# Performance work log

Hardware: AMD Instinct MI355X
Metric: run time of the kernel (lower is better)

## Reference

```python
import jax, jax.numpy as jnp
import numpy as np

B, SQ, SKV = 4, 2048, 2048
IN_Q, IN_KV = 1024, 1024
H, D = 16, 64            # num_heads, hidden_channels (per-head dim)
OUT = 1024
ROPE_BASE = 4096.0


def _rope(x, base):
    # x: (..., items, D). Interleaved rotate-half RoPE over last dim.
    d = x.shape[-1]
    s = x.shape[-2]
    inv_freq = base ** (-jnp.arange(0, d, 2, dtype=x.dtype) / d)      # (D/2,)
    ang = jnp.arange(s, dtype=x.dtype)[:, None] * inv_freq[None, :]   # (S, D/2)
    cos = jnp.repeat(jnp.cos(ang), 2, axis=-1)                        # (S, D)
    sin = jnp.repeat(jnp.sin(ang), 2, axis=-1)
    xp = x.reshape(x.shape[:-1] + (d // 2, 2))
    x_rot = jnp.stack([-xp[..., 1], xp[..., 0]], axis=-1).reshape(x.shape)
    return x * cos + x_rot * sin


def setup_inputs() -> dict:
    key = jax.random.key(0)
    ks = jax.random.split(key, 8)
    sc = 0.02
    return {
        "q": jax.random.normal(ks[0], (B, SQ, IN_Q), jnp.float32),
        "kv": jax.random.normal(ks[1], (B, SKV, IN_KV), jnp.float32),
        # weights stored (in, out): y = x @ W + b  (equiv. to torch Linear)
        "Wq": jax.random.normal(ks[2], (IN_Q, H * D), jnp.float32) * sc,
        "bq": jnp.zeros((H * D,), jnp.float32),
        "Wkv": jax.random.normal(ks[3], (IN_KV, 2 * D), jnp.float32) * sc,
        "bkv": jnp.zeros((2 * D,), jnp.float32),
        "Wo": jax.random.normal(ks[4], (H * D, OUT), jnp.float32) * sc,
        "bo": jnp.zeros((OUT,), jnp.float32),
    }


def reference(q, kv, Wq, bq, Wkv, bkv, Wo, bo):
    # Q projection -> (B, H, SQ, D)
    qh = (q @ Wq + bq).reshape(B, SQ, H, D).transpose(0, 2, 1, 3)
    # KV projection (multi-query: single shared K/V head) -> (B, SKV, D) each
    kvp = kv @ Wkv + bkv
    k, v = kvp[..., :D], kvp[..., D:]
    # Rotary positional encoding on the item axis
    qh = _rope(qh, ROPE_BASE)
    k = _rope(k, ROPE_BASE)
    # Scaled dot-product attention with broadcast single-head K/V (MQA)
    scale = 1.0 / jnp.sqrt(jnp.asarray(D, qh.dtype))
    scores = jnp.einsum("bhqd,bkd->bhqk", qh, k) * scale   # (B,H,SQ,SKV)
    attn = jax.nn.softmax(scores, axis=-1)
    h = jnp.einsum("bhqk,bkd->bhqd", attn, v)              # (B,H,SQ,D)
    # Merge heads and output projection
    h = h.transpose(0, 2, 1, 3).reshape(B, SQ, H * D)
    return h @ Wo + bo
```

## Files before the change

### kernel.cpp

```cpp
#include <hip/hip_runtime.h>
#include <math.h>

typedef __bf16 bf16;
typedef __bf16 bf16x4 __attribute__((ext_vector_type(4)));
typedef __bf16 bf16x8 __attribute__((ext_vector_type(8)));
typedef float floatx4 __attribute__((ext_vector_type(4)));

#define MFMA16(a, b, c) __builtin_amdgcn_mfma_f32_16x16x32_bf16(a, b, c, 0, 0, 0)

#if __has_builtin(__builtin_amdgcn_exp2f)
#define EXP2F(x) __builtin_amdgcn_exp2f(x)
#else
#define EXP2F(x) exp2f(x)
#endif

constexpr int Bc = 4, SQc = 2048, SKVc = 2048, Hc = 16, Dc = 64;
#define QSCALE 0.18033688011112042f

__device__ __forceinline__ void glds16(const bf16* g, bf16* lds_base, int lane) {
#if __has_builtin(__builtin_amdgcn_global_load_lds)
  __builtin_amdgcn_global_load_lds(
      (const __attribute__((address_space(1))) void*)g,
      (__attribute__((address_space(3))) void*)lds_base, 16, 0, 0);
#else
  *(bf16x8*)(lds_base + 8 * lane) = *(const bf16x8*)g;
#endif
}

__device__ __forceinline__ void cvt_body(const float* __restrict__ in,
                                         bf16* __restrict__ out, int blk,
                                         int tid) {
  const size_t i = ((size_t)blk * 256 + tid) * 4;
  const float4 v = *(const float4*)&in[i];
  bf16x4 o = {(bf16)v.x, (bf16)v.y, (bf16)v.z, (bf16)v.w};
  *(bf16x4*)&out[i] = o;
}

__device__ __forceinline__ void transpose_body(const float* __restrict__ in,
                                               bf16* __restrict__ out, int K,
                                               int N, int bx, int by, int tid,
                                               bf16 (*T)[72]) {
  const int n0 = bx * 64, k0 = by * 64;
  const int tr = tid >> 4, tc4 = (tid & 15) * 4;
#pragma unroll
  for (int i = 0; i < 4; i++) {
    const int k = tr + 16 * i;
    const float4 v = *(const float4*)&in[(size_t)(k0 + k) * N + n0 + tc4];
    T[tc4 + 0][k] = (bf16)v.x;
    T[tc4 + 1][k] = (bf16)v.y;
    T[tc4 + 2][k] = (bf16)v.z;
    T[tc4 + 3][k] = (bf16)v.w;
  }
  __syncthreads();
  const int nr = tid >> 2, kc = (tid & 3) * 8;
#pragma unroll
  for (int hf = 0; hf < 2; hf++)
    *(bf16x8*)&out[(size_t)(n0 + nr) * K + k0 + kc + 32 * hf] =
        *(const bf16x8*)&T[nr][kc + 32 * hf];
}

__global__ void prep(const float* __restrict__ q, const float* __restrict__ kv,
                     const float* __restrict__ Wq, const float* __restrict__ Wkv,
                     const float* __restrict__ Wo, bf16* __restrict__ qbf,
                     bf16* __restrict__ kvbf, bf16* __restrict__ WqT,
                     bf16* __restrict__ WkvT, bf16* __restrict__ WoT,
                     float2* __restrict__ rtab) {
  __shared__ bf16 T[64][72];
  const int blk = blockIdx.x, tid = threadIdx.x;
  if (blk < 8192) {
    cvt_body(q, qbf, blk, tid);
  } else if (blk < 16384) {
    cvt_body(kv, kvbf, blk - 8192, tid);
  } else if (blk < 16640) {
    const int i = blk - 16384;
    transpose_body(Wq, WqT, 1024, 1024, i & 15, i >> 4, tid, T);
  } else if (blk < 16672) {
    const int i = blk - 16640;
    transpose_body(Wkv, WkvT, 1024, 128, i & 1, i >> 1, tid, T);
  } else if (blk < 16928) {
    const int i = blk - 16672;
    transpose_body(Wo, WoT, 1024, 1024, i & 15, i >> 4, tid, T);
  } else {
    const int i = (blk - 16928) * 256 + tid;
    const int pos = i >> 5, f = i & 31;
    const float ang = (float)pos * exp2f(-0.375f * (float)f);
    float sn, cs;
    sincosf(ang, &sn, &cs);
    rtab[i] = make_float2(cs, sn);
  }
}

__device__ __forceinline__ void gemm_kloop(const bf16* __restrict__ A,
                                           const bf16* __restrict__ BT, int m0,
                                           int n0, int tid, int wave, int lane,
                                           int m, int g, bf16* As, bf16* Bs,
                                           floatx4 (*acc)[2], int mq, int nq) {
  const int r_ = tid >> 3, p_ = tid & 7;
  const bf16* pA[4];
  const bf16* pB[2];
#pragma unroll
  for (int q = 0; q < 4; q++) {
    const int r = r_ + q * 32;
    const int s = p_ ^ (r & 7);
    pA[q] = &A[(size_t)(m0 + r) * 1024 + 8 * s];
    if (q < 2) pB[q] = &BT[(size_t)(n0 + r) * 1024 + 8 * s];
  }

  for (int k0 = 0; k0 < 1024; k0 += 64) {
    __syncthreads();
#pragma unroll
    for (int q = 0; q < 4; q++)
      glds16(pA[q] + k0, &As[(q * 4 + wave) * 512], lane);
#pragma unroll
    for (int q = 0; q < 2; q++)
      glds16(pB[q] + k0, &Bs[(q * 4 + wave) * 512], lane);
    __syncthreads();

    bf16x8 bb[2][2];
#pragma unroll
    for (int j = 0; j < 2; j++) {
      const int row = nq + 16 * j + m;
#pragma unroll
      for (int kh = 0; kh < 2; kh++)
        bb[j][kh] = *(const bf16x8*)&Bs[row * 64 + 8 * ((g + 4 * kh) ^ (row & 7))];
    }
#pragma unroll
    for (int i = 0; i < 4; i++) {
      const int row = mq + 16 * i + m;
      const bf16x8 a0 = *(const bf16x8*)&As[row * 64 + 8 * (g ^ (row & 7))];
      const bf16x8 a1 = *(const bf16x8*)&As[row * 64 + 8 * ((g + 4) ^ (row & 7))];
#pragma unroll
      for (int j = 0; j < 2; j++) {
        acc[i][j] = MFMA16(a0, bb[j][0], acc[i][j]);
        acc[i][j] = MFMA16(a1, bb[j][1], acc[i][j]);
      }
    }
  }
}

__global__ __launch_bounds__(256, 4) void gemm_qkv(
    const bf16* __restrict__ qA, const bf16* __restrict__ qBT,
    const float* __restrict__ qb, const bf16* __restrict__ kvA,
    const bf16* __restrict__ kvBT, const float* __restrict__ kvb,
    const float2* __restrict__ tab, bf16* __restrict__ qh,
    bf16* __restrict__ kko, bf16* __restrict__ vto) {
  __shared__ bf16 As[128 * 64];
  __shared__ bf16 Bs[64 * 64];

  const int tid = threadIdx.x, lane = tid & 63, wave = tid >> 6;
  const int m = lane & 15, g = lane >> 4;
  const int m0 = blockIdx.x * 128;
  const bool isQ = (blockIdx.y < 16);
  const int n0 = isQ ? blockIdx.y * 64 : (blockIdx.y - 16) * 64;
  const bf16* A = isQ ? qA : kvA;
  const bf16* BT = isQ ? qBT : kvBT;
  const float* bias = isQ ? qb : kvb;
  const int mq = (wave >> 1) * 64, nq = (wave & 1) * 32;

  floatx4 z = {0.f, 0.f, 0.f, 0.f};
  floatx4 acc[4][2];
#pragma unroll
  for (int i = 0; i < 4; i++)
#pragma unroll
    for (int j = 0; j < 2; j++) acc[i][j] = z;

  gemm_kloop(A, BT, m0, n0, tid, wave, lane, m, g, As, Bs, acc, mq, nq);

  const int rq = 4 * g;
#pragma unroll
  for (int j = 0; j < 2; j++) {
    const int col = n0 + nq + 16 * j + m;
    const float bv = bias[col];
#pragma unroll
    for (int i = 0; i < 4; i++) {
#pragma unroll
      for (int r = 0; r < 4; r++) {
        const int row = m0 + mq + 16 * i + rq + r;
        float v = acc[i][j][r] + bv;
        const float vp = __shfl_xor(v, 1);
        if (isQ) {
          const int d = col & 63, hh = col >> 6;
          const int pos = row & (SQc - 1), b = row >> 11;
          const float2 cssn = tab[pos * 32 + (d >> 1)];
          const float res = (d & 1) ? (v * cssn.x + vp * cssn.y)
                                    : (v * cssn.x - vp * cssn.y);
          qh[(((size_t)(b * Hc + hh) * SQc) + pos) * Dc + d] = (bf16)(res * QSCALE);
        } else {
          const int pos = row & (SKVc - 1), b = row >> 11;
          const size_t fb = (size_t)b * (SKVc * Dc);
          if (col < 64) {
            const int d = col;
            const float2 cssn = tab[pos * 32 + (d >> 1)];
            const float res = (d & 1) ? (v * cssn.x + vp * cssn.y)
                                      : (v * cssn.x - vp * cssn.y);
            const int kc = (pos >> 4) * 2 + (d >> 5);
            const int kl = ((d >> 3) & 3) * 16 + (pos & 15);
            kko[fb + (size_t)kc * 512 + kl * 8 + (d & 7)] = (bf16)res;
          } else {
            const int d = col - 64;
            const int vc = (pos >> 6) * 8 + (d >> 4) * 2 + ((pos >> 5) & 1);
            const int vl = ((pos >> 3) & 3) * 16 + (d & 15);
            vto[fb + (size_t)vc * 512 + vl * 8 + (pos & 7)] = (bf16)v;
          }
        }
      }
    }
  }
}

__global__ __launch_bounds__(256, 4) void gemm_out(
    const bf16* __restrict__ A, const bf16* __restrict__ BT,
    const float* __restrict__ bias, float* __restrict__ out) {
  __shared__ bf16 As[128 * 64];
  __shared__ bf16 Bs[64 * 64];

  const int tid = threadIdx.x, lane = tid & 63, wave = tid >> 6;
  const int m = lane & 15, g = lane >> 4;
  const int m0 = blockIdx.x * 128, n0 = blockIdx.y * 64;
  const int mq = (wave >> 1) * 64, nq = (wave & 1) * 32;

  floatx4 z = {0.f, 0.f, 0.f, 0.f};
  floatx4 acc[4][2];
#pragma unroll
  for (int i = 0; i < 4; i++)
#pragma unroll
    for (int j = 0; j < 2; j++) acc[i][j] = z;

  gemm_kloop(A, BT, m0, n0, tid, wave, lane, m, g, As, Bs, acc, mq, nq);

  const int rq = 4 * g;
#pragma unroll
  for (int j = 0; j < 2; j++) {
    const int col = n0 + nq + 16 * j + m;
    const float bv = bias[col];
#pragma unroll
    for (int i = 0; i < 4; i++)
#pragma unroll
      for (int r = 0; r < 4; r++) {
        const int row = m0 + mq + 16 * i + rq + r;
        out[(size_t)row * 1024 + col] = acc[i][j][r] + bv;
      }
  }
}

__global__ __launch_bounds__(512, 4) void attn_v5(
    const bf16* __restrict__ qh, const bf16* __restrict__ kk,
    const bf16* __restrict__ vt, bf16* __restrict__ hout) {
  const int bid = blockIdx.x;
  const int qt = bid & 7, h = (bid >> 3) & 15, b = bid >> 7;
  const int tid = threadIdx.x, lane = tid & 63, wave = tid >> 6;
  const int m = lane & 15, g = lane >> 4;

  __shared__ bf16 Kb[2][4096];
  __shared__ bf16 Vb[4096];
  __shared__ bf16 Pb[8][2][16][68];

  const int q0 = qt * 256 + wave * 32;
  const bf16* qp = qh + (((size_t)(b * Hc + h) * SQc) + q0 + m) * Dc + 8 * g;
  bf16x8 bq[2][2];
#pragma unroll
  for (int s = 0; s < 2; s++) {
    bq[s][0] = *(const bf16x8*)(qp + (size_t)(16 * s) * Dc);
    bq[s][1] = *(const bf16x8*)(qp + (size_t)(16 * s) * Dc + 32);
  }

  const bf16 one = (bf16)1.0f;
  const bf16x8 ones = {one, one, one, one, one, one, one, one};

  floatx4 z = {0.f, 0.f, 0.f, 0.f};
  floatx4 accO[2][4];
  floatx4 lacc[2] = {z, z};
#pragma unroll
  for (int s = 0; s < 2; s++)
#pragma unroll
    for (int t = 0; t < 4; t++) accO[s][t] = z;

  const size_t fb = (size_t)b * (SKVc * Dc);
  const bf16* kg = kk + fb + 8 * lane;
  const bf16* vg = vt + fb + 8 * lane;

  glds16(kg + (size_t)wave * 512, &Kb[0][wave * 512], lane);
  __syncthreads();

  for (int it = 0; it < 32; ++it) {
    const int cur = it & 1;
    if (it) __syncthreads();
    glds16(vg + (size_t)(it * 8 + wave) * 512, &Vb[wave * 512], lane);
    if (it + 1 < 32)
      glds16(kg + (size_t)((it + 1) * 8 + wave) * 512, &Kb[cur ^ 1][wave * 512],
             lane);

    bf16x8 kfr[4][2];
#pragma unroll
    for (int c = 0; c < 4; c++) {
      kfr[c][0] = *(const bf16x8*)&Kb[cur][(2 * c + 0) * 512 + 8 * lane];
      kfr[c][1] = *(const bf16x8*)&Kb[cur][(2 * c + 1) * 512 + 8 * lane];
    }
#pragma unroll
    for (int s = 0; s < 2; s++) {
#pragma unroll
      for (int c = 0; c < 4; c++) {
        floatx4 sv = MFMA16(kfr[c][0], bq[s][0], z);
        sv = MFMA16(kfr[c][1], bq[s][1], sv);
        bf16x4 pk = {(bf16)EXP2F(sv[0]), (bf16)EXP2F(sv[1]), (bf16)EXP2F(sv[2]),
                     (bf16)EXP2F(sv[3])};
        *(bf16x4*)&Pb[wave][s][m][16 * c + 4 * g] = pk;
      }
    }
    __syncthreads();

    bf16x8 vf[4][2];
#pragma unroll
    for (int t = 0; t < 4; t++) {
      vf[t][0] = *(const bf16x8*)&Vb[(2 * t + 0) * 512 + 8 * lane];
      vf[t][1] = *(const bf16x8*)&Vb[(2 * t + 1) * 512 + 8 * lane];
    }
    __builtin_amdgcn_s_setprio(1);
#pragma unroll
    for (int s = 0; s < 2; s++) {
      const bf16x8 pa0 = *(const bf16x8*)&Pb[wave][s][m][8 * g];
      const bf16x8 pa1 = *(const bf16x8*)&Pb[wave][s][m][32 + 8 * g];
      lacc[s] = MFMA16(pa0, ones, lacc[s]);
      lacc[s] = MFMA16(pa1, ones, lacc[s]);
#pragma unroll
      for (int t = 0; t < 4; t++) {
        accO[s][t] = MFMA16(pa0, vf[t][0], accO[s][t]);
        accO[s][t] = MFMA16(pa1, vf[t][1], accO[s][t]);
      }
    }
    __builtin_amdgcn_s_setprio(0);
  }

#pragma unroll
  for (int s = 0; s < 2; s++) {
    floatx4 inv;
#pragma unroll
    for (int r = 0; r < 4; r++) inv[r] = 1.0f / lacc[s][r];
#pragma unroll
    for (int t = 0; t < 4; t++)
#pragma unroll
      for (int r = 0; r < 4; r++) {
        const int qrow = q0 + 16 * s + 4 * g + r;
        hout[((size_t)(b * SQc + qrow)) * (Hc * Dc) + h * Dc + 16 * t + m] =
            (bf16)(accO[s][t][r] * inv[r]);
      }
  }
}

extern "C" void kernel_launch(void* const* d_in, const int* in_sizes, int n_in,
                              void* d_out, int out_size, void* d_ws, size_t ws_size,
                              hipStream_t stream) {
  const float* q = (const float*)d_in[0];
  const float* kv = (const float*)d_in[1];
  const float* Wq = (const float*)d_in[2];
  const float* bq = (const float*)d_in[3];
  const float* Wkv = (const float*)d_in[4];
  const float* bkv = (const float*)d_in[5];
  const float* Wo = (const float*)d_in[6];
  const float* bo = (const float*)d_in[7];

  char* ws = (char*)d_ws;
  bf16* qbf = (bf16*)ws;
  bf16* kvbf = (bf16*)(ws + ((size_t)16 << 20));
  bf16* WqT = (bf16*)(ws + ((size_t)32 << 20));
  bf16* WkvT = (bf16*)(ws + ((size_t)34 << 20));
  float2* rtab = (float2*)(ws + ((size_t)34 << 20) + ((size_t)256 << 10));
  bf16* WoT = (bf16*)(ws + ((size_t)35 << 20));
  bf16* qh = (bf16*)(ws + ((size_t)37 << 20));
  bf16* kk = (bf16*)(ws + ((size_t)53 << 20));
  bf16* vt = (bf16*)(ws + ((size_t)54 << 20));
  bf16* hh = qbf;

  prep<<<17184, 256, 0, stream>>>(q, kv, Wq, Wkv, Wo, qbf, kvbf, WqT, WkvT, WoT,
                                  rtab);
  gemm_qkv<<<dim3(64, 18), 256, 0, stream>>>(qbf, WqT, bq, kvbf, WkvT, bkv, rtab,
                                             qh, kk, vt);
  attn_v5<<<Bc * Hc * (SQc / 256), 512, 0, stream>>>(qh, kk, vt, hh);
  gemm_out<<<dim3(64, 16), 256, 0, stream>>>(hh, WoT, bo, (float*)d_out);
}
```

Baseline: 261.5 us.

## Enlarge GEMM tiles to 256x64 with K-step 128 and 512-thread blocks

Both projection GEMMs now use 256-row by 64-column block tiles with a K depth of 128 per stage and 8 waves per block. Each wave owns 32 rows and all 64 columns, with a 16-wide XOR swizzle in LDS. This halves the number of K-loop barriers and raises the reuse of each B tile, so global-to-LDS traffic per FLOP drops. In exchange LDS use grows to 80KB per block and the grid shrinks to 576 and 512 blocks, which lowers occupancy and may leave CUs idle.

```diff
diff --git a/kernel.cpp b/kernel.cpp
--- a/kernel.cpp
+++ b/kernel.cpp
@@ -94,88 +94,80 @@
                                            const bf16* __restrict__ BT, int m0,
                                            int n0, int tid, int wave, int lane,
                                            int m, int g, bf16* As, bf16* Bs,
-                                           floatx4 (*acc)[2], int mq, int nq) {
-  const int r_ = tid >> 3, p_ = tid & 7;
-  const bf16* pA[4];
-  const bf16* pB[2];
-#pragma unroll
-  for (int q = 0; q < 4; q++) {
-    const int r = r_ + q * 32;
-    const int s = p_ ^ (r & 7);
-    pA[q] = &A[(size_t)(m0 + r) * 1024 + 8 * s];
-    if (q < 2) pB[q] = &BT[(size_t)(n0 + r) * 1024 + 8 * s];
-  }
-
-  for (int k0 = 0; k0 < 1024; k0 += 64) {
+                                           floatx4 (*acc)[4]) {
+  const int r_ = tid >> 4, p_ = tid & 15;
+  const int sw = p_ ^ (r_ & 15);
+  const bf16* pA0 = &A[(size_t)(m0 + r_) * 1024 + 8 * sw];
+  const bf16* pB0 = &BT[(size_t)(n0 + r_) * 1024 + 8 * sw];
+
+  for (int k0 = 0; k0 < 1024; k0 += 128) {
     __syncthreads();
 #pragma unroll
-    for (int q = 0; q < 4; q++)
-      glds16(pA[q] + k0, &As[(q * 4 + wave) * 512], lane);
+    for (int q = 0; q < 8; q++)
+      glds16(pA0 + (size_t)q * 32 * 1024 + k0, &As[(q * 8 + wave) * 512], lane);
 #pragma unroll
     for (int q = 0; q < 2; q++)
-      glds16(pB[q] + k0, &Bs[(q * 4 + wave) * 512], lane);
+      glds16(pB0 + (size_t)q * 32 * 1024 + k0, &Bs[(q * 8 + wave) * 512], lane);
     __syncthreads();
 
-    bf16x8 bb[2][2];
-#pragma unroll
-    for (int j = 0; j < 2; j++) {
-      const int row = nq + 16 * j + m;
-#pragma unroll
-      for (int kh = 0; kh < 2; kh++)
-        bb[j][kh] = *(const bf16x8*)&Bs[row * 64 + 8 * ((g + 4 * kh) ^ (row & 7))];
-    }
-#pragma unroll
-    for (int i = 0; i < 4; i++) {
-      const int row = mq + 16 * i + m;
-      const bf16x8 a0 = *(const bf16x8*)&As[row * 64 + 8 * (g ^ (row & 7))];
-      const bf16x8 a1 = *(const bf16x8*)&As[row * 64 + 8 * ((g + 4) ^ (row & 7))];
-#pragma unroll
-      for (int j = 0; j < 2; j++) {
-        acc[i][j] = MFMA16(a0, bb[j][0], acc[i][j]);
-        acc[i][j] = MFMA16(a1, bb[j][1], acc[i][j]);
-      }
-    }
-  }
-}
-
-__global__ __launch_bounds__(256, 4) void gemm_qkv(
+#pragma unroll
+    for (int ks = 0; ks < 4; ks++) {
+      bf16x8 af[2], bfr[4];
+#pragma unroll
+      for (int i = 0; i < 2; i++) {
+        const int row = wave * 32 + 16 * i + m;
+        af[i] = *(const bf16x8*)&As[row * 128 + 8 * ((4 * ks + g) ^ (row & 15))];
+      }
+#pragma unroll
+      for (int j = 0; j < 4; j++) {
+        const int row = 16 * j + m;
+        bfr[j] = *(const bf16x8*)&Bs[row * 128 + 8 * ((4 * ks + g) ^ (row & 15))];
+      }
+#pragma unroll
+      for (int i = 0; i < 2; i++)
+#pragma unroll
+        for (int j = 0; j < 4; j++) acc[i][j] = MFMA16(af[i], bfr[j], acc[i][j]);
+    }
+  }
+}
+
+__global__ __launch_bounds__(512, 2) void gemm_qkv(
     const bf16* __restrict__ qA, const bf16* __restrict__ qBT,
     const float* __restrict__ qb, const bf16* __restrict__ kvA,
     const bf16* __restrict__ kvBT, const float* __restrict__ kvb,
     const float2* __restrict__ tab, bf16* __restrict__ qh,
     bf16* __restrict__ kko, bf16* __restrict__ vto) {
-  __shared__ bf16 As[128 * 64];
-  __shared__ bf16 Bs[64 * 64];
+  __shared__ bf16 As[256 * 128];
+  __shared__ bf16 Bs[64 * 128];
 
   const int tid = threadIdx.x, lane = tid & 63, wave = tid >> 6;
   const int m = lane & 15, g = lane >> 4;
-  const int m0 = blockIdx.x * 128;
+  const int m0 = blockIdx.x * 256;
   const bool isQ = (blockIdx.y < 16);
   const int n0 = isQ ? blockIdx.y * 64 : (blockIdx.y - 16) * 64;
   const bf16* A = isQ ? qA : kvA;
   const bf16* BT = isQ ? qBT : kvBT;
   const float* bias = isQ ? qb : kvb;
-  const int mq = (wave >> 1) * 64, nq = (wave & 1) * 32;
 
   floatx4 z = {0.f, 0.f, 0.f, 0.f};
-  floatx4 acc[4][2];
-#pragma unroll
-  for (int i = 0; i < 4; i++)
-#pragma unroll
-    for (int j = 0; j < 2; j++) acc[i][j] = z;
-
-  gemm_kloop(A, BT, m0, n0, tid, wave, lane, m, g, As, Bs, acc, mq, nq);
+  floatx4 acc[2][4];
+#pragma unroll
+  for (int i = 0; i < 2; i++)
+#pragma unroll
+    for (int j = 0; j < 4; j++) acc[i][j] = z;
+
+  gemm_kloop(A, BT, m0, n0, tid, wave, lane, m, g, As, Bs, acc);
 
   const int rq = 4 * g;
 #pragma unroll
-  for (int j = 0; j < 2; j++) {
-    const int col = n0 + nq + 16 * j + m;
+  for (int j = 0; j < 4; j++) {
+    const int col = n0 + 16 * j + m;
     const float bv = bias[col];
 #pragma unroll
-    for (int i = 0; i < 4; i++) {
+    for (int i = 0; i < 2; i++) {
 #pragma unroll
       for (int r = 0; r < 4; r++) {
-        const int row = m0 + mq + 16 * i + rq + r;
+        const int row = m0 + wave * 32 + 16 * i + rq + r;
         float v = acc[i][j][r] + bv;
         const float vp = __shfl_xor(v, 1);
         if (isQ) {
@@ -208,36 +200,35 @@
   }
 }
 
-__global__ __launch_bounds__(256, 4) void gemm_out(
+__global__ __launch_bounds__(512, 2) void gemm_out(
     const bf16* __restrict__ A, const bf16* __restrict__ BT,
     const float* __restrict__ bias, float* __restrict__ out) {
-  __shared__ bf16 As[128 * 64];
-  __shared__ bf16 Bs[64 * 64];
+  __shared__ bf16 As[256 * 128];
+  __shared__ bf16 Bs[64 * 128];
 
   const int tid = threadIdx.x, lane = tid & 63, wave = tid >> 6;
   const int m = lane & 15, g = lane >> 4;
-  const int m0 = blockIdx.x * 128, n0 = blockIdx.y * 64;
-  const int mq = (wave >> 1) * 64, nq = (wave & 1) * 32;
+  const int m0 = blockIdx.x * 256, n0 = blockIdx.y * 64;
 
   floatx4 z = {0.f, 0.f, 0.f, 0.f};
-  floatx4 acc[4][2];
-#pragma unroll
-  for (int i = 0; i < 4; i++)
-#pragma unroll
-    for (int j = 0; j < 2; j++) acc[i][j] = z;
-
-  gemm_kloop(A, BT, m0, n0, tid, wave, lane, m, g, As, Bs, acc, mq, nq);
+  floatx4 acc[2][4];
+#pragma unroll
+  for (int i = 0; i < 2; i++)
+#pragma unroll
+    for (int j = 0; j < 4; j++) acc[i][j] = z;
+
+  gemm_kloop(A, BT, m0, n0, tid, wave, lane, m, g, As, Bs, acc);
 
   const int rq = 4 * g;
 #pragma unroll
-  for (int j = 0; j < 2; j++) {
-    const int col = n0 + nq + 16 * j + m;
+  for (int j = 0; j < 4; j++) {
+    const int col = n0 + 16 * j + m;
     const float bv = bias[col];
 #pragma unroll
-    for (int i = 0; i < 4; i++)
+    for (int i = 0; i < 2; i++)
 #pragma unroll
       for (int r = 0; r < 4; r++) {
-        const int row = m0 + mq + 16 * i + rq + r;
+        const int row = m0 + wave * 32 + 16 * i + rq + r;
         out[(size_t)row * 1024 + col] = acc[i][j][r] + bv;
       }
   }
@@ -373,8 +364,8 @@
 
   prep<<<17184, 256, 0, stream>>>(q, kv, Wq, Wkv, Wo, qbf, kvbf, WqT, WkvT, WoT,
                                   rtab);
-  gemm_qkv<<<dim3(64, 18), 256, 0, stream>>>(qbf, WqT, bq, kvbf, WkvT, bkv, rtab,
+  gemm_qkv<<<dim3(32, 18), 512, 0, stream>>>(qbf, WqT, bq, kvbf, WkvT, bkv, rtab,
                                              qh, kk, vt);
   attn_v5<<<Bc * Hc * (SQc / 256), 512, 0, stream>>>(qh, kk, vt, hh);
-  gemm_out<<<dim3(64, 16), 256, 0, stream>>>(hh, WoT, bo, (float*)d_out);
-}
+  gemm_out<<<dim3(32, 16), 512, 0, stream>>>(hh, WoT, bo, (float*)d_out);
+}
```

After: 264.9 us. Within noise of the previous version (+1.3%).
